# Performance work log

Hardware: AMD Instinct MI355X
Metric: run time of the kernel (lower is better)

Reference implementation:

```python
import jax, jax.numpy as jnp
import numpy as np


def _conv1x1(W, b, x):
    # 1x1 conv == per-pixel matmul over channels: (O,C) x (B,C,H,W) -> (B,O,H,W)
    return jnp.einsum('oc,bchw->bohw', W, x) + b[None, :, None, None]


def setup_inputs() -> dict:
    key = jax.random.key(0)
    ks = jax.random.split(key, 7)
    B, C, H, W = 4, 256, 64, 64
    Cq = C // 8  # 32
    scale_qk = 1.0 / np.sqrt(C)
    x = jax.random.normal(ks[0], (B, C, H, W), dtype=jnp.float32)
    Wq = jax.random.normal(ks[1], (Cq, C), dtype=jnp.float32) * scale_qk
    bq = jnp.zeros((Cq,), dtype=jnp.float32)
    Wk = jax.random.normal(ks[2], (Cq, C), dtype=jnp.float32) * scale_qk
    bk = jnp.zeros((Cq,), dtype=jnp.float32)
    Wv = jax.random.normal(ks[3], (C, C), dtype=jnp.float32) * scale_qk
    bv = jnp.zeros((C,), dtype=jnp.float32)
    gamma = jnp.ones((1,), dtype=jnp.float32)  # torch init is 0; use 1 so attn branch is exercised
    return {'x': x, 'Wq': Wq, 'bq': bq, 'Wk': Wk, 'bk': bk, 'Wv': Wv, 'bv': bv, 'gamma': gamma}


def reference(x, Wq, bq, Wk, bk, Wv, bv, gamma):
    B, C, H, W = x.shape
    N = H * W
    # query/key projections + activation (relu), flattened over spatial dims
    q = jax.nn.relu(_conv1x1(Wq, bq, x)).reshape(B, -1, N)  # (B, C/8, N)
    k = jax.nn.relu(_conv1x1(Wk, bk, x)).reshape(B, -1, N)  # (B, C/8, N)
    # energy[b,n,m] = sum_c q[b,c,n] * k[b,c,m]  (= proj_query^T @ proj_key)
    energy = jnp.einsum('bcn,bcm->bnm', q, k)               # (B, N, N)
    attention = jax.nn.softmax(energy, axis=-1)
    v = jax.nn.relu(_conv1x1(Wv, bv, x)).reshape(B, C, N)   # (B, C, N)
    # out = v @ attention^T : out[b,c,n] = sum_m v[b,c,m] * attention[b,n,m]
    out = jnp.einsum('bcm,bnm->bcn', v, attention).reshape(B, C, H, W)
    out = gamma[0] * out + x
    return (out, attention)
```

## Files before the change

kernel.cpp:

```cpp
#include <hip/hip_runtime.h>
#include <hip/hip_bf16.h>

#define NB 4
#define NC 256
#define NQ 32
#define NN 4096

typedef __attribute__((ext_vector_type(4))) float f32x4;
typedef __attribute__((ext_vector_type(8))) short s16x8;

__device__ __forceinline__ float bf2f(short s) {
    return __uint_as_float(((unsigned int)(unsigned short)s) << 16);
}
#define MFMA16(a, b, c) __builtin_amdgcn_mfma_f32_16x16x32_bf16((a), (b), (c), 0, 0, 0)

__device__ __forceinline__ void block_sync_lds() {
    asm volatile("s_waitcnt lgkmcnt(0)" ::: "memory");
    __builtin_amdgcn_s_barrier();
}

__device__ __forceinline__ int pswz(int row, int col) {
    return row * 64 + (col ^ ((row & 7) << 3));
}

__global__ __launch_bounds__(512, 2) void k_proj(
    const float* __restrict__ x,
    const float* __restrict__ Wq, const float* __restrict__ bq,
    const float* __restrict__ Wk, const float* __restrict__ bk,
    const float* __restrict__ Wv, const float* __restrict__ bv,
    __hip_bfloat16* __restrict__ qh, __hip_bfloat16* __restrict__ ql,
    __hip_bfloat16* __restrict__ kh, __hip_bfloat16* __restrict__ kl,
    __hip_bfloat16* __restrict__ vo)
{
    __shared__ __align__(16) float xs[NC * 64];
    const int b  = blockIdx.y;
    const int n0 = blockIdx.x * 64;
    const int t  = threadIdx.x;

    {
        const float* xb = x + (size_t)b * NC * NN + n0;
        #pragma unroll
        for (int it = 0; it < 8; ++it) {
            int i4 = t + it * 512;
            int c  = i4 >> 4;
            int nq = (i4 & 15) << 2;
            float4 v4 = *(const float4*)(xb + (size_t)c * NN + nq);
            *(float4*)&xs[c * 64 + nq] = v4;
        }
    }
    __syncthreads();

    const int g  = t >> 4;
    const int n4 = (t & 15) << 2;

    const float* Wr[10];
    float a[10][4];
    #pragma unroll
    for (int j = 0; j < 10; ++j) {
        int o = g + 32 * j;
        const float* Wrow; float bias;
        if (o < 32)      { Wrow = Wq + o * NC;        bias = bq[o]; }
        else if (o < 64) { Wrow = Wk + (o - 32) * NC; bias = bk[o - 32]; }
        else             { Wrow = Wv + (o - 64) * NC; bias = bv[o - 64]; }
        Wr[j] = Wrow;
        a[j][0] = a[j][1] = a[j][2] = a[j][3] = bias;
    }

    #pragma unroll 2
    for (int c0 = 0; c0 < NC; c0 += 4) {
        float4 xv[4];
        #pragma unroll
        for (int i = 0; i < 4; ++i) xv[i] = *(const float4*)&xs[(c0 + i) * 64 + n4];
        #pragma unroll
        for (int j = 0; j < 10; ++j) {
            float4 w = *(const float4*)(Wr[j] + c0);
            a[j][0] += w.x * xv[0].x + w.y * xv[1].x + w.z * xv[2].x + w.w * xv[3].x;
            a[j][1] += w.x * xv[0].y + w.y * xv[1].y + w.z * xv[2].y + w.w * xv[3].y;
            a[j][2] += w.x * xv[0].z + w.y * xv[1].z + w.z * xv[2].z + w.w * xv[3].z;
            a[j][3] += w.x * xv[0].w + w.y * xv[1].w + w.z * xv[2].w + w.w * xv[3].w;
        }
    }

    #pragma unroll
    for (int j = 0; j < 10; ++j) {
        int o = g + 32 * j;
        float a0 = fmaxf(a[j][0], 0.f), a1 = fmaxf(a[j][1], 0.f);
        float a2 = fmaxf(a[j][2], 0.f), a3 = fmaxf(a[j][3], 0.f);
        int nn = n0 + n4;
        if (o < 64) {
            __hip_bfloat16 *dh, *dl; int c;
            if (o < 32) { dh = qh; dl = ql; c = o; }
            else        { dh = kh; dl = kl; c = o - 32; }
            float vals[4] = {a0, a1, a2, a3};
            #pragma unroll
            for (int i = 0; i < 4; ++i) {
                float vv = vals[i];
                __hip_bfloat16 h = __float2bfloat16(vv);
                float lo = vv - __bfloat162float(h);
                size_t base = ((size_t)b * NN + nn + i) * NQ + c;
                dh[base] = h;
                dl[base] = __float2bfloat16(lo);
            }
        } else {
            union { __hip_bfloat16 h[4]; unsigned long long u; } pk;
            pk.h[0] = __float2bfloat16(a0); pk.h[1] = __float2bfloat16(a1);
            pk.h[2] = __float2bfloat16(a2); pk.h[3] = __float2bfloat16(a3);
            *(unsigned long long*)(vo + ((size_t)b * NC + (o - 64)) * NN + nn) = pk.u;
        }
    }
}

__global__ __launch_bounds__(512, 2) void k_fused(
    const __hip_bfloat16* __restrict__ qh, const __hip_bfloat16* __restrict__ ql,
    const __hip_bfloat16* __restrict__ kh, const __hip_bfloat16* __restrict__ kl,
    const __hip_bfloat16* __restrict__ v,
    const float* __restrict__ x, const float* __restrict__ gamma,
    float* __restrict__ out, float* __restrict__ att)
{
    __shared__ __align__(16) __hip_bfloat16 ps[2][64 * 64];
    __shared__ float redM[8][16], redS[8][16];
    __shared__ float finM[64], finI[64];

    const int flat = blockIdx.y * 64 + blockIdx.x;
    const int swzb = (flat & 7) * 32 + (flat >> 3);
    const int b  = swzb >> 6;
    const int n0 = (swzb & 63) * 64;

    const int t = threadIdx.x, wv = t >> 6, lane = t & 63;
    const int r = lane & 15, hi = lane >> 4, kc = hi * 8;
    const int wq = wv & 3;
    const int nw = n0 + wq * 16;

    const __hip_bfloat16* khb = kh + (size_t)b * NN * NQ;
    const __hip_bfloat16* klb = kl + (size_t)b * NN * NQ;
    const __hip_bfloat16* vb  = v  + (size_t)b * NC * NN;

    s16x8 aqh = *(const s16x8*)(qh + ((size_t)b * NN + nw + r) * NQ + kc);
    s16x8 aql = *(const s16x8*)(ql + ((size_t)b * NN + nw + r) * NQ + kc);

    float M[4], S[4];
    #pragma unroll
    for (int j = 0; j < 4; ++j) { M[j] = -3.0e38f; S[j] = 0.f; }
    {
        const int hb = (wv >> 2) * (NN / 2);
        s16x8 c0h = *(const s16x8*)(khb + (size_t)(hb + r) * NQ + kc);
        s16x8 c0l = *(const s16x8*)(klb + (size_t)(hb + r) * NQ + kc);
        s16x8 c1h = *(const s16x8*)(khb + (size_t)(hb + 16 + r) * NQ + kc);
        s16x8 c1l = *(const s16x8*)(klb + (size_t)(hb + 16 + r) * NQ + kc);
        #pragma unroll 1
        for (int it = 0; it < 64; ++it) {
            s16x8 u0h = c0h, u0l = c0l, u1h = c1h, u1l = c1l;
            if (it < 63) {
                int m = hb + (it + 1) * 32;
                c0h = *(const s16x8*)(khb + (size_t)(m + r) * NQ + kc);
                c0l = *(const s16x8*)(klb + (size_t)(m + r) * NQ + kc);
                c1h = *(const s16x8*)(khb + (size_t)(m + 16 + r) * NQ + kc);
                c1l = *(const s16x8*)(klb + (size_t)(m + 16 + r) * NQ + kc);
            }
            f32x4 e0 = {0.f, 0.f, 0.f, 0.f}, e1 = {0.f, 0.f, 0.f, 0.f};
            e0 = MFMA16(aqh, u0h, e0); e0 = MFMA16(aqh, u0l, e0); e0 = MFMA16(aql, u0h, e0);
            e1 = MFMA16(aqh, u1h, e1); e1 = MFMA16(aqh, u1l, e1); e1 = MFMA16(aql, u1h, e1);
            #pragma unroll
            for (int j = 0; j < 4; ++j) {
                float v0 = e0[j], v1 = e1[j];
                float nm = fmaxf(M[j], fmaxf(v0, v1));
                S[j] = S[j] * __expf(M[j] - nm) + __expf(v0 - nm) + __expf(v1 - nm);
                M[j] = nm;
            }
        }
    }
    #pragma unroll
    for (int off = 1; off < 16; off <<= 1) {
        #pragma unroll
        for (int j = 0; j < 4; ++j) {
            float M2 = __shfl_xor(M[j], off), S2 = __shfl_xor(S[j], off);
            float nm = fmaxf(M[j], M2);
            S[j] = S[j] * __expf(M[j] - nm) + S2 * __expf(M2 - nm);
            M[j] = nm;
        }
    }
    if (r == 0) {
        #pragma unroll
        for (int j = 0; j < 4; ++j) { redM[wv][hi * 4 + j] = M[j]; redS[wv][hi * 4 + j] = S[j]; }
    }
    __syncthreads();
    if (t < 64) {
        int tw = t >> 4, tl = t & 15;
        float M1 = redM[tw][tl], M2 = redM[tw + 4][tl];
        float Mf = fmaxf(M1, M2);
        float Sf = redS[tw][tl] * __expf(M1 - Mf) + redS[tw + 4][tl] * __expf(M2 - Mf);
        finM[t] = Mf; finI[t] = 1.0f / Sf;
    }
    __syncthreads();

    if (wv < 4) {
        float fM[4], fI[4];
        #pragma unroll
        for (int j = 0; j < 4; ++j) {
            fM[j] = finM[wq * 16 + hi * 4 + j];
            fI[j] = finI[wq * 16 + hi * 4 + j];
        }
        float* abase = att + ((size_t)b * NN + nw + r) * NN;
        const int rl = wq * 16 + r;

        s16x8 c0h = *(const s16x8*)(khb + (size_t)(r) * NQ + kc);
        s16x8 c0l = *(const s16x8*)(klb + (size_t)(r) * NQ + kc);
        s16x8 c1h = *(const s16x8*)(khb + (size_t)(16 + r) * NQ + kc);
        s16x8 c1l = *(const s16x8*)(klb + (size_t)(16 + r) * NQ + kc);

        #pragma unroll 1
        for (int st = 0; st < 64; ++st) {
            const int m0 = st * 64, buf = st & 1;
            #pragma unroll
            for (int ch = 0; ch < 2; ++ch) {
                s16x8 u0h = c0h, u0l = c0l, u1h = c1h, u1l = c1l;
                int mn = m0 + ch * 32 + 32;
                if (mn < NN) {
                    c0h = *(const s16x8*)(khb + (size_t)(mn + r) * NQ + kc);
                    c0l = *(const s16x8*)(klb + (size_t)(mn + r) * NQ + kc);
                    c1h = *(const s16x8*)(khb + (size_t)(mn + 16 + r) * NQ + kc);
                    c1l = *(const s16x8*)(klb + (size_t)(mn + 16 + r) * NQ + kc);
                }
                f32x4 e0 = {0.f, 0.f, 0.f, 0.f}, e1 = {0.f, 0.f, 0.f, 0.f};
                e0 = MFMA16(aqh, u0h, e0); e0 = MFMA16(aqh, u0l, e0); e0 = MFMA16(aql, u0h, e0);
                e1 = MFMA16(aqh, u1h, e1); e1 = MFMA16(aqh, u1l, e1); e1 = MFMA16(aql, u1h, e1);
                #pragma unroll
                for (int j = 0; j < 4; ++j) {
                    float p0 = __expf(e0[j] - fM[j]) * fI[j];
                    float p1 = __expf(e1[j] - fM[j]) * fI[j];
                    int row = wq * 16 + hi * 4 + j;
                    ps[buf][pswz(row, ch * 32 + r)]      = __float2bfloat16(p0);
                    ps[buf][pswz(row, ch * 32 + 16 + r)] = __float2bfloat16(p1);
                }
            }
            #pragma unroll
            for (int ch = 0; ch < 2; ++ch) {
                s16x8 pf = *(const s16x8*)&ps[buf][pswz(rl, ch * 32 + kc)];
                f32x4 w0, w1;
                w0[0] = bf2f(pf[0]); w0[1] = bf2f(pf[1]); w0[2] = bf2f(pf[2]); w0[3] = bf2f(pf[3]);
                w1[0] = bf2f(pf[4]); w1[1] = bf2f(pf[5]); w1[2] = bf2f(pf[6]); w1[3] = bf2f(pf[7]);
                __builtin_nontemporal_store(w0, (f32x4*)(abase + m0 + ch * 32 + kc));
                __builtin_nontemporal_store(w1, (f32x4*)(abase + m0 + ch * 32 + kc + 4));
            }
            block_sync_lds();
        }
    } else {
        const int cw = (wv - 4) * 64;
        f32x4 acc[4][4] = {};
        s16x8 vA[4], vB[4];
        #pragma unroll
        for (int ct = 0; ct < 4; ++ct)
            vA[ct] = *(const s16x8*)(vb + (size_t)(cw + ct * 16 + r) * NN + kc);

        #pragma unroll 1
        for (int st = 0; st < 64; ++st) {
            if (st > 0) {
                const int cst = st - 1, pb = cst & 1, mP = cst * 64;
                #pragma unroll
                for (int ct = 0; ct < 4; ++ct)
                    vB[ct] = *(const s16x8*)(vb + (size_t)(cw + ct * 16 + r) * NN + mP + 32 + kc);
                s16x8 pf0[4];
                #pragma unroll
                for (int nt = 0; nt < 4; ++nt)
                    pf0[nt] = *(const s16x8*)&ps[pb][pswz(nt * 16 + r, kc)];
                __builtin_amdgcn_s_setprio(1);
                #pragma unroll
                for (int ct = 0; ct < 4; ++ct)
                    #pragma unroll
                    for (int nt = 0; nt < 4; ++nt)
                        acc[ct][nt] = MFMA16(vA[ct], pf0[nt], acc[ct][nt]);
                __builtin_amdgcn_s_setprio(0);
                if (cst < 63) {
                    #pragma unroll
                    for (int ct = 0; ct < 4; ++ct)
                        vA[ct] = *(const s16x8*)(vb + (size_t)(cw + ct * 16 + r) * NN + mP + 64 + kc);
                }
                s16x8 pf1[4];
                #pragma unroll
                for (int nt = 0; nt < 4; ++nt)
                    pf1[nt] = *(const s16x8*)&ps[pb][pswz(nt * 16 + r, 32 + kc)];
                __builtin_amdgcn_s_setprio(1);
                #pragma unroll
                for (int ct = 0; ct < 4; ++ct)
                    #pragma unroll
                    for (int nt = 0; nt < 4; ++nt)
                        acc[ct][nt] = MFMA16(vB[ct], pf1[nt], acc[ct][nt]);
                __builtin_amdgcn_s_setprio(0);
            }
            block_sync_lds();
        }
        {
            const int pb = 1, mP = 63 * 64;
            #pragma unroll
            for (int ct = 0; ct < 4; ++ct)
                vB[ct] = *(const s16x8*)(vb + (size_t)(cw + ct * 16 + r) * NN + mP + 32 + kc);
            s16x8 pf0[4], pf1[4];
            #pragma unroll
            for (int nt = 0; nt < 4; ++nt) {
                pf0[nt] = *(const s16x8*)&ps[pb][pswz(nt * 16 + r, kc)];
                pf1[nt] = *(const s16x8*)&ps[pb][pswz(nt * 16 + r, 32 + kc)];
            }
            #pragma unroll
            for (int ct = 0; ct < 4; ++ct)
                #pragma unroll
                for (int nt = 0; nt < 4; ++nt) {
                    acc[ct][nt] = MFMA16(vA[ct], pf0[nt], acc[ct][nt]);
                    acc[ct][nt] = MFMA16(vB[ct], pf1[nt], acc[ct][nt]);
                }
        }
        const float gm = gamma[0];
        #pragma unroll
        for (int ct = 0; ct < 4; ++ct) {
            #pragma unroll
            for (int nt = 0; nt < 4; ++nt) {
                #pragma unroll
                for (int j = 0; j < 4; ++j) {
                    int c = cw + ct * 16 + hi * 4 + j;
                    size_t idx = ((size_t)b * NC + c) * NN + n0 + nt * 16 + r;
                    out[idx] = gm * acc[ct][nt][j] + x[idx];
                }
            }
        }
    }
}

extern "C" void kernel_launch(void* const* d_in, const int* in_sizes, int n_in,
                              void* d_out, int out_size, void* d_ws, size_t ws_size,
                              hipStream_t stream) {
    const float* x     = (const float*)d_in[0];
    const float* Wq    = (const float*)d_in[1];
    const float* bq    = (const float*)d_in[2];
    const float* Wk    = (const float*)d_in[3];
    const float* bk    = (const float*)d_in[4];
    const float* Wv    = (const float*)d_in[5];
    const float* bv    = (const float*)d_in[6];
    const float* gamma = (const float*)d_in[7];

    float* out = (float*)d_out;
    float* att = out + (size_t)NB * NC * NN;

    const size_t qk_elems = (size_t)NB * NN * NQ;
    __hip_bfloat16* qh = (__hip_bfloat16*)d_ws;
    __hip_bfloat16* ql = qh + qk_elems;
    __hip_bfloat16* kh = ql + qk_elems;
    __hip_bfloat16* kl = kh + qk_elems;
    __hip_bfloat16* vo = kl + qk_elems;

    k_proj <<<dim3(NN / 64, NB), 512, 0, stream>>>(x, Wq, bq, Wk, bk, Wv, bv,
                                                   qh, ql, kh, kl, vo);
    k_fused<<<dim3(NN / 64, NB), 512, 0, stream>>>(qh, ql, kh, kl, vo,
                                                   x, gamma, out, att);
}
```

Baseline: 223.0 us.

## Restructure fused attention kernel to 1024 threads with exp2 softmax and swapped MFMA operands

The fused kernel now launches 1024-thread blocks. Eight waves compute attention rows and eight waves compute the value product, instead of four and four. The first softmax pass splits the key range four ways per row tile. MFMA operand order is swapped so each lane holds one query row, which allows per-lane scalar max/sum and direct float4 attention stores without the LDS bf16 round-trip. The softmax uses raw v_exp_f32 with log2(e) folded into the q projection. Attention stores now come straight from fp32 values instead of being reread from bf16 LDS, which changes the attention output precision. The cost is higher register pressure at launch bounds (1024,4).

```diff
diff --git a/kernel.cpp b/kernel.cpp
--- a/kernel.cpp
+++ b/kernel.cpp
@@ -5,14 +5,18 @@
 #define NC 256
 #define NQ 32
 #define NN 4096
+#define LOG2E 1.4426950408889634f
 
 typedef __attribute__((ext_vector_type(4))) float f32x4;
 typedef __attribute__((ext_vector_type(8))) short s16x8;
 
-__device__ __forceinline__ float bf2f(short s) {
-    return __uint_as_float(((unsigned int)(unsigned short)s) << 16);
-}
 #define MFMA16(a, b, c) __builtin_amdgcn_mfma_f32_16x16x32_bf16((a), (b), (c), 0, 0, 0)
+
+__device__ __forceinline__ float fexp2(float x) {
+    float r;
+    asm("v_exp_f32 %0, %1" : "=v"(r) : "v"(x));
+    return r;
+}
 
 __device__ __forceinline__ void block_sync_lds() {
     asm volatile("s_waitcnt lgkmcnt(0)" ::: "memory");
@@ -88,10 +92,10 @@
         float a2 = fmaxf(a[j][2], 0.f), a3 = fmaxf(a[j][3], 0.f);
         int nn = n0 + n4;
         if (o < 64) {
-            __hip_bfloat16 *dh, *dl; int c;
-            if (o < 32) { dh = qh; dl = ql; c = o; }
-            else        { dh = kh; dl = kl; c = o - 32; }
-            float vals[4] = {a0, a1, a2, a3};
+            __hip_bfloat16 *dh, *dl; int c; float sc;
+            if (o < 32) { dh = qh; dl = ql; c = o;      sc = LOG2E; }
+            else        { dh = kh; dl = kl; c = o - 32; sc = 1.0f;  }
+            float vals[4] = {a0 * sc, a1 * sc, a2 * sc, a3 * sc};
             #pragma unroll
             for (int i = 0; i < 4; ++i) {
                 float vv = vals[i];
@@ -110,7 +114,7 @@
     }
 }
 
-__global__ __launch_bounds__(512, 2) void k_fused(
+__global__ __launch_bounds__(1024, 4) void k_fused(
     const __hip_bfloat16* __restrict__ qh, const __hip_bfloat16* __restrict__ ql,
     const __hip_bfloat16* __restrict__ kh, const __hip_bfloat16* __restrict__ kl,
     const __hip_bfloat16* __restrict__ v,
@@ -118,199 +122,190 @@
     float* __restrict__ out, float* __restrict__ att)
 {
     __shared__ __align__(16) __hip_bfloat16 ps[2][64 * 64];
-    __shared__ float redM[8][16], redS[8][16];
+    __shared__ float redM[16][16], redS[16][16];
     __shared__ float finM[64], finI[64];
 
-    const int flat = blockIdx.y * 64 + blockIdx.x;
-    const int swzb = (flat & 7) * 32 + (flat >> 3);
-    const int b  = swzb >> 6;
-    const int n0 = (swzb & 63) * 64;
+    const int bid  = blockIdx.x;
+    const int flat = (bid & 7) * 32 + (bid >> 3);
+    const int b    = flat >> 6;
+    const int n0   = (flat & 63) * 64;
 
     const int t = threadIdx.x, wv = t >> 6, lane = t & 63;
     const int r = lane & 15, hi = lane >> 4, kc = hi * 8;
-    const int wq = wv & 3;
-    const int nw = n0 + wq * 16;
 
     const __hip_bfloat16* khb = kh + (size_t)b * NN * NQ;
     const __hip_bfloat16* klb = kl + (size_t)b * NN * NQ;
     const __hip_bfloat16* vb  = v  + (size_t)b * NC * NN;
 
-    s16x8 aqh = *(const s16x8*)(qh + ((size_t)b * NN + nw + r) * NQ + kc);
-    s16x8 aql = *(const s16x8*)(ql + ((size_t)b * NN + nw + r) * NQ + kc);
-
-    float M[4], S[4];
-    #pragma unroll
-    for (int j = 0; j < 4; ++j) { M[j] = -3.0e38f; S[j] = 0.f; }
     {
-        const int hb = (wv >> 2) * (NN / 2);
-        s16x8 c0h = *(const s16x8*)(khb + (size_t)(hb + r) * NQ + kc);
-        s16x8 c0l = *(const s16x8*)(klb + (size_t)(hb + r) * NQ + kc);
-        s16x8 c1h = *(const s16x8*)(khb + (size_t)(hb + 16 + r) * NQ + kc);
-        s16x8 c1l = *(const s16x8*)(klb + (size_t)(hb + 16 + r) * NQ + kc);
+        const int nt1 = wv >> 2, mq = wv & 3;
+        const int nw = n0 + nt1 * 16;
+        const s16x8 aqh = *(const s16x8*)(qh + ((size_t)b * NN + nw + r) * NQ + kc);
+        const s16x8 aql = *(const s16x8*)(ql + ((size_t)b * NN + nw + r) * NQ + kc);
+        const int mb = mq * 1024;
+        float M = -3.0e38f, S = 0.f;
+        s16x8 c0h = *(const s16x8*)(khb + (size_t)(mb + r) * NQ + kc);
+        s16x8 c0l = *(const s16x8*)(klb + (size_t)(mb + r) * NQ + kc);
+        s16x8 c1h = *(const s16x8*)(khb + (size_t)(mb + 16 + r) * NQ + kc);
+        s16x8 c1l = *(const s16x8*)(klb + (size_t)(mb + 16 + r) * NQ + kc);
         #pragma unroll 1
-        for (int it = 0; it < 64; ++it) {
+        for (int it = 0; it < 32; ++it) {
             s16x8 u0h = c0h, u0l = c0l, u1h = c1h, u1l = c1l;
-            if (it < 63) {
-                int m = hb + (it + 1) * 32;
+            if (it < 31) {
+                int m = mb + (it + 1) * 32;
                 c0h = *(const s16x8*)(khb + (size_t)(m + r) * NQ + kc);
                 c0l = *(const s16x8*)(klb + (size_t)(m + r) * NQ + kc);
                 c1h = *(const s16x8*)(khb + (size_t)(m + 16 + r) * NQ + kc);
                 c1l = *(const s16x8*)(klb + (size_t)(m + 16 + r) * NQ + kc);
             }
             f32x4 e0 = {0.f, 0.f, 0.f, 0.f}, e1 = {0.f, 0.f, 0.f, 0.f};
-            e0 = MFMA16(aqh, u0h, e0); e0 = MFMA16(aqh, u0l, e0); e0 = MFMA16(aql, u0h, e0);
-            e1 = MFMA16(aqh, u1h, e1); e1 = MFMA16(aqh, u1l, e1); e1 = MFMA16(aql, u1h, e1);
-            #pragma unroll
-            for (int j = 0; j < 4; ++j) {
-                float v0 = e0[j], v1 = e1[j];
-                float nm = fmaxf(M[j], fmaxf(v0, v1));
-                S[j] = S[j] * __expf(M[j] - nm) + __expf(v0 - nm) + __expf(v1 - nm);
-                M[j] = nm;
-            }
-        }
-    }
-    #pragma unroll
-    for (int off = 1; off < 16; off <<= 1) {
-        #pragma unroll
-        for (int j = 0; j < 4; ++j) {
-            float M2 = __shfl_xor(M[j], off), S2 = __shfl_xor(S[j], off);
-            float nm = fmaxf(M[j], M2);
-            S[j] = S[j] * __expf(M[j] - nm) + S2 * __expf(M2 - nm);
-            M[j] = nm;
-        }
-    }
-    if (r == 0) {
-        #pragma unroll
-        for (int j = 0; j < 4; ++j) { redM[wv][hi * 4 + j] = M[j]; redS[wv][hi * 4 + j] = S[j]; }
+            e0 = MFMA16(u0h, aqh, e0); e0 = MFMA16(u0l, aqh, e0); e0 = MFMA16(u0h, aql, e0);
+            e1 = MFMA16(u1h, aqh, e1); e1 = MFMA16(u1l, aqh, e1); e1 = MFMA16(u1h, aql, e1);
+            float mx = fmaxf(fmaxf(fmaxf(e0[0], e0[1]), fmaxf(e0[2], e0[3])),
+                             fmaxf(fmaxf(e1[0], e1[1]), fmaxf(e1[2], e1[3])));
+            float nm = fmaxf(M, mx);
+            float s8 = fexp2(e0[0] - nm) + fexp2(e0[1] - nm) +
+                       fexp2(e0[2] - nm) + fexp2(e0[3] - nm) +
+                       fexp2(e1[0] - nm) + fexp2(e1[1] - nm) +
+                       fexp2(e1[2] - nm) + fexp2(e1[3] - nm);
+            S = S * fexp2(M - nm) + s8;
+            M = nm;
+        }
+        #pragma unroll
+        for (int off = 16; off <= 32; off <<= 1) {
+            float M2 = __shfl_xor(M, off), S2 = __shfl_xor(S, off);
+            float nm = fmaxf(M, M2);
+            S = S * fexp2(M - nm) + S2 * fexp2(M2 - nm);
+            M = nm;
+        }
+        if (lane < 16) { redM[wv][r] = M; redS[wv][r] = S; }
     }
     __syncthreads();
     if (t < 64) {
-        int tw = t >> 4, tl = t & 15;
-        float M1 = redM[tw][tl], M2 = redM[tw + 4][tl];
-        float Mf = fmaxf(M1, M2);
-        float Sf = redS[tw][tl] * __expf(M1 - Mf) + redS[tw + 4][tl] * __expf(M2 - Mf);
-        finM[t] = Mf; finI[t] = 1.0f / Sf;
+        const int w0 = (t >> 4) * 4, tl = t & 15;
+        float M = redM[w0][tl], S = redS[w0][tl];
+        #pragma unroll
+        for (int i = 1; i < 4; ++i) {
+            float M2 = redM[w0 + i][tl], S2 = redS[w0 + i][tl];
+            float nm = fmaxf(M, M2);
+            S = S * fexp2(M - nm) + S2 * fexp2(M2 - nm);
+            M = nm;
+        }
+        finM[t] = M; finI[t] = 1.0f / S;
     }
     __syncthreads();
 
-    if (wv < 4) {
-        float fM[4], fI[4];
-        #pragma unroll
-        for (int j = 0; j < 4; ++j) {
-            fM[j] = finM[wq * 16 + hi * 4 + j];
-            fI[j] = finI[wq * 16 + hi * 4 + j];
-        }
-        float* abase = att + ((size_t)b * NN + nw + r) * NN;
-        const int rl = wq * 16 + r;
-
-        s16x8 c0h = *(const s16x8*)(khb + (size_t)(r) * NQ + kc);
-        s16x8 c0l = *(const s16x8*)(klb + (size_t)(r) * NQ + kc);
-        s16x8 c1h = *(const s16x8*)(khb + (size_t)(16 + r) * NQ + kc);
-        s16x8 c1l = *(const s16x8*)(klb + (size_t)(16 + r) * NQ + kc);
+    if (wv < 8) {
+        const int nt = wv >> 1, mh = wv & 1;
+        const int nw = n0 + nt * 16;
+        const s16x8 aqh = *(const s16x8*)(qh + ((size_t)b * NN + nw + r) * NQ + kc);
+        const s16x8 aql = *(const s16x8*)(ql + ((size_t)b * NN + nw + r) * NQ + kc);
+        const float fM = finM[nt * 16 + r], fI = finI[nt * 16 + r];
+        float* arow = att + ((size_t)b * NN + nw + r) * NN;
+        const int prow = nt * 16 + r;
+        const int pc0  = mh * 32 + hi * 4;
+
+        int mt = mh * 32;
+        s16x8 c0h = *(const s16x8*)(khb + (size_t)(mt + r) * NQ + kc);
+        s16x8 c0l = *(const s16x8*)(klb + (size_t)(mt + r) * NQ + kc);
+        s16x8 c1h = *(const s16x8*)(khb + (size_t)(mt + 16 + r) * NQ + kc);
+        s16x8 c1l = *(const s16x8*)(klb + (size_t)(mt + 16 + r) * NQ + kc);
 
         #pragma unroll 1
         for (int st = 0; st < 64; ++st) {
-            const int m0 = st * 64, buf = st & 1;
-            #pragma unroll
-            for (int ch = 0; ch < 2; ++ch) {
-                s16x8 u0h = c0h, u0l = c0l, u1h = c1h, u1l = c1l;
-                int mn = m0 + ch * 32 + 32;
-                if (mn < NN) {
-                    c0h = *(const s16x8*)(khb + (size_t)(mn + r) * NQ + kc);
-                    c0l = *(const s16x8*)(klb + (size_t)(mn + r) * NQ + kc);
-                    c1h = *(const s16x8*)(khb + (size_t)(mn + 16 + r) * NQ + kc);
-                    c1l = *(const s16x8*)(klb + (size_t)(mn + 16 + r) * NQ + kc);
-                }
-                f32x4 e0 = {0.f, 0.f, 0.f, 0.f}, e1 = {0.f, 0.f, 0.f, 0.f};
-                e0 = MFMA16(aqh, u0h, e0); e0 = MFMA16(aqh, u0l, e0); e0 = MFMA16(aql, u0h, e0);
-                e1 = MFMA16(aqh, u1h, e1); e1 = MFMA16(aqh, u1l, e1); e1 = MFMA16(aql, u1h, e1);
-                #pragma unroll
-                for (int j = 0; j < 4; ++j) {
-                    float p0 = __expf(e0[j] - fM[j]) * fI[j];
-                    float p1 = __expf(e1[j] - fM[j]) * fI[j];
-                    int row = wq * 16 + hi * 4 + j;
-                    ps[buf][pswz(row, ch * 32 + r)]      = __float2bfloat16(p0);
-                    ps[buf][pswz(row, ch * 32 + 16 + r)] = __float2bfloat16(p1);
-                }
-            }
-            #pragma unroll
-            for (int ch = 0; ch < 2; ++ch) {
-                s16x8 pf = *(const s16x8*)&ps[buf][pswz(rl, ch * 32 + kc)];
-                f32x4 w0, w1;
-                w0[0] = bf2f(pf[0]); w0[1] = bf2f(pf[1]); w0[2] = bf2f(pf[2]); w0[3] = bf2f(pf[3]);
-                w1[0] = bf2f(pf[4]); w1[1] = bf2f(pf[5]); w1[2] = bf2f(pf[6]); w1[3] = bf2f(pf[7]);
-                __builtin_nontemporal_store(w0, (f32x4*)(abase + m0 + ch * 32 + kc));
-                __builtin_nontemporal_store(w1, (f32x4*)(abase + m0 + ch * 32 + kc + 4));
-            }
+            const int buf = st & 1;
+            s16x8 u0h = c0h, u0l = c0l, u1h = c1h, u1l = c1l;
+            if (st < 63) {
+                int mn = mt + 64;
+                c0h = *(const s16x8*)(khb + (size_t)(mn + r) * NQ + kc);
+                c0l = *(const s16x8*)(klb + (size_t)(mn + r) * NQ + kc);
+                c1h = *(const s16x8*)(khb + (size_t)(mn + 16 + r) * NQ + kc);
+                c1l = *(const s16x8*)(klb + (size_t)(mn + 16 + r) * NQ + kc);
+            }
+            f32x4 e0 = {0.f, 0.f, 0.f, 0.f}, e1 = {0.f, 0.f, 0.f, 0.f};
+            e0 = MFMA16(u0h, aqh, e0); e0 = MFMA16(u0l, aqh, e0); e0 = MFMA16(u0h, aql, e0);
+            e1 = MFMA16(u1h, aqh, e1); e1 = MFMA16(u1l, aqh, e1); e1 = MFMA16(u1h, aql, e1);
+
+            f32x4 w0, w1;
+            #pragma unroll
+            for (int j = 0; j < 4; ++j) {
+                w0[j] = fexp2(e0[j] - fM) * fI;
+                w1[j] = fexp2(e1[j] - fM) * fI;
+            }
+            __builtin_nontemporal_store(w0, (f32x4*)(arow + mt + hi * 4));
+            __builtin_nontemporal_store(w1, (f32x4*)(arow + mt + 16 + hi * 4));
+            union { __hip_bfloat16 h[4]; unsigned long long u; } pk0, pk1;
+            #pragma unroll
+            for (int j = 0; j < 4; ++j) {
+                pk0.h[j] = __float2bfloat16(w0[j]);
+                pk1.h[j] = __float2bfloat16(w1[j]);
+            }
+            *(unsigned long long*)&ps[buf][pswz(prow, pc0)]      = pk0.u;
+            *(unsigned long long*)&ps[buf][pswz(prow, pc0 + 16)] = pk1.u;
+
             block_sync_lds();
+            mt += 64;
         }
     } else {
-        const int cw = (wv - 4) * 64;
-        f32x4 acc[4][4] = {};
-        s16x8 vA[4], vB[4];
-        #pragma unroll
-        for (int ct = 0; ct < 4; ++ct)
-            vA[ct] = *(const s16x8*)(vb + (size_t)(cw + ct * 16 + r) * NN + kc);
+        const int cw = (wv - 8) * 32;
+        f32x4 acc[2][4] = {};
 
         #pragma unroll 1
         for (int st = 0; st < 64; ++st) {
             if (st > 0) {
                 const int cst = st - 1, pb = cst & 1, mP = cst * 64;
-                #pragma unroll
-                for (int ct = 0; ct < 4; ++ct)
-                    vB[ct] = *(const s16x8*)(vb + (size_t)(cw + ct * 16 + r) * NN + mP + 32 + kc);
-                s16x8 pf0[4];
+                s16x8 vf0[2], vf1[2], pf0[4], pf1[4];
+                #pragma unroll
+                for (int ct = 0; ct < 2; ++ct)
+                    vf0[ct] = *(const s16x8*)(vb + (size_t)(cw + ct * 16 + r) * NN + mP + kc);
                 #pragma unroll
                 for (int nt = 0; nt < 4; ++nt)
                     pf0[nt] = *(const s16x8*)&ps[pb][pswz(nt * 16 + r, kc)];
-                __builtin_amdgcn_s_setprio(1);
-                #pragma unroll
-                for (int ct = 0; ct < 4; ++ct)
-                    #pragma unroll
-                    for (int nt = 0; nt < 4; ++nt)
-                        acc[ct][nt] = MFMA16(vA[ct], pf0[nt], acc[ct][nt]);
-                __builtin_amdgcn_s_setprio(0);
-                if (cst < 63) {
-                    #pragma unroll
-                    for (int ct = 0; ct < 4; ++ct)
-                        vA[ct] = *(const s16x8*)(vb + (size_t)(cw + ct * 16 + r) * NN + mP + 64 + kc);
-                }
-                s16x8 pf1[4];
+                #pragma unroll
+                for (int ct = 0; ct < 2; ++ct)
+                    vf1[ct] = *(const s16x8*)(vb + (size_t)(cw + ct * 16 + r) * NN + mP + 32 + kc);
                 #pragma unroll
                 for (int nt = 0; nt < 4; ++nt)
                     pf1[nt] = *(const s16x8*)&ps[pb][pswz(nt * 16 + r, 32 + kc)];
                 __builtin_amdgcn_s_setprio(1);
                 #pragma unroll
-                for (int ct = 0; ct < 4; ++ct)
+                for (int ct = 0; ct < 2; ++ct)
                     #pragma unroll
                     for (int nt = 0; nt < 4; ++nt)
-                        acc[ct][nt] = MFMA16(vB[ct], pf1[nt], acc[ct][nt]);
+                        acc[ct][nt] = MFMA16(vf0[ct], pf0[nt], acc[ct][nt]);
+                #pragma unroll
+                for (int ct = 0; ct < 2; ++ct)
+                    #pragma unroll
+                    for (int nt = 0; nt < 4; ++nt)
+                        acc[ct][nt] = MFMA16(vf1[ct], pf1[nt], acc[ct][nt]);
                 __builtin_amdgcn_s_setprio(0);
             }
             block_sync_lds();
         }
         {
-            const int pb = 1, mP = 63 * 64;
-            #pragma unroll
-            for (int ct = 0; ct < 4; ++ct)
-                vB[ct] = *(const s16x8*)(vb + (size_t)(cw + ct * 16 + r) * NN + mP + 32 + kc);
-            s16x8 pf0[4], pf1[4];
+            const int mP = 63 * 64;
+            s16x8 vf0[2], vf1[2], pf0[4], pf1[4];
+            #pragma unroll
+            for (int ct = 0; ct < 2; ++ct) {
+                vf0[ct] = *(const s16x8*)(vb + (size_t)(cw + ct * 16 + r) * NN + mP + kc);
+                vf1[ct] = *(const s16x8*)(vb + (size_t)(cw + ct * 16 + r) * NN + mP + 32 + kc);
+            }
             #pragma unroll
             for (int nt = 0; nt < 4; ++nt) {
-                pf0[nt] = *(const s16x8*)&ps[pb][pswz(nt * 16 + r, kc)];
-                pf1[nt] = *(const s16x8*)&ps[pb][pswz(nt * 16 + r, 32 + kc)];
-            }
-            #pragma unroll
-            for (int ct = 0; ct < 4; ++ct)
+                pf0[nt] = *(const s16x8*)&ps[1][pswz(nt * 16 + r, kc)];
+                pf1[nt] = *(const s16x8*)&ps[1][pswz(nt * 16 + r, 32 + kc)];
+            }
+            #pragma unroll
+            for (int ct = 0; ct < 2; ++ct)
                 #pragma unroll
                 for (int nt = 0; nt < 4; ++nt) {
-                    acc[ct][nt] = MFMA16(vA[ct], pf0[nt], acc[ct][nt]);
-                    acc[ct][nt] = MFMA16(vB[ct], pf1[nt], acc[ct][nt]);
+                    acc[ct][nt] = MFMA16(vf0[ct], pf0[nt], acc[ct][nt]);
+                    acc[ct][nt] = MFMA16(vf1[ct], pf1[nt], acc[ct][nt]);
                 }
         }
         const float gm = gamma[0];
         #pragma unroll
-        for (int ct = 0; ct < 4; ++ct) {
+        for (int ct = 0; ct < 2; ++ct) {
             #pragma unroll
             for (int nt = 0; nt < 4; ++nt) {
                 #pragma unroll
@@ -348,6 +343,6 @@
 
     k_proj <<<dim3(NN / 64, NB), 512, 0, stream>>>(x, Wq, bq, Wk, bk, Wv, bv,
                                                    qh, ql, kh, kl, vo);
-    k_fused<<<dim3(NN / 64, NB), 512, 0, stream>>>(qh, ql, kh, kl, vo,
-                                                   x, gamma, out, att);
-}
+    k_fused<<<dim3(256), 1024, 0, stream>>>(qh, ql, kh, kl, vo,
+                                            x, gamma, out, att);
+}
```

After: 202.3 us. 9.3% less time.
